# Kernel tuning notes

Hardware: AMD Instinct MI355X
Metric: run time of the kernel (lower is better)

The kernel has to match this reference:

```python
import jax, jax.numpy as jnp
import numpy as np

N, D = 100000, 256   # nodes, out_dim
E = N - 1            # chain dependency graph: gov[i]=i -> dep[i]=i+1
NEG = jnp.float32(-1e18)
LEAKY_SLOPE = 0.2    # __init__ alpha


def setup_inputs() -> dict:
    key = jax.random.key(0)
    k1, k2, k3 = jax.random.split(key, 3)
    x = jax.random.normal(k1, (N, D), dtype=jnp.float32)
    W = jax.random.normal(k2, (D, D), dtype=jnp.float32) / np.float32(np.sqrt(D))
    a = jax.random.normal(k3, (2 * D,), dtype=jnp.float32) / np.float32(np.sqrt(2 * D))
    gov = jnp.arange(E, dtype=jnp.int32)      # governors 0..N-2
    dep = jnp.arange(E, dtype=jnp.int32) + 1  # dependents 1..N-1 (each unique)
    return {"x": x, "W": W, "a": a, "gov": gov, "dep": dep}


def reference(x, W, a, gov, dep):
    n, d = x.shape
    h = x @ W.T                                   # [N, D]  W x_v for all nodes
    a_gov, a_dep = a[:d], a[d:]
    # per-edge score: attn_weight(cat(W x_gov, W x_dep))
    s = h[gov] @ a_gov + h[dep] @ a_dep           # [E]
    # original: masked_e = where(row > 0, row, -1e18); softmax over full row of N.
    # Non-edge entries are 0 -> masked to -1e18. In fp32 exp(-1e18 - rowmax)
    # underflows to 0 whenever rowmax > -1e18, so the dense softmax reduces to a
    # segment softmax over positive edge scores; if all row entries are masked,
    # softmax is uniform 1/N.
    sm = jnp.where(s > 0, s, NEG)
    rowmax = jax.ops.segment_max(sm, gov, num_segments=n)
    rowmax = jnp.maximum(rowmax, NEG)             # non-edge entries are -1e18
    ex = jnp.exp(sm - rowmax[gov])                # [E]
    deg = jax.ops.segment_sum(jnp.ones_like(s), gov, num_segments=n)
    denom = jax.ops.segment_sum(ex, gov, num_segments=n) \
          + (jnp.float32(n) - deg) * jnp.exp(NEG - rowmax)
    alpha = ex / denom[gov]                       # [E] attention coefficients
    # self_loop: h_dict[dep] = W x_gov (dep unique -> simple scatter-set); node 0 -> zeros
    base = jnp.zeros_like(h).at[dep].set(h[gov])
    # aggregation: h_dict[gov] += alpha * W x_dep
    out = base.at[gov].add(alpha[:, None] * h[dep])
    # is_dropout=False path: leakyrelu only (dropout is stochastic, eval mode)
    return jax.nn.leaky_relu(out, negative_slope=LEAKY_SLOPE)
```

## Files before the change

### kernel.cpp

```cpp
#include <hip/hip_runtime.h>

#define NR   100000
#define DD   256
#define BMO  62
#define HR   64
#define NCH  1613
#define GRID 256
#define LDA  72
#define LDH  264

typedef unsigned short u16;
typedef __bf16 bf16_t;
typedef bf16_t bf16x8 __attribute__((ext_vector_type(8)));
typedef float  f32x4  __attribute__((ext_vector_type(4)));
typedef u16    u16x8  __attribute__((ext_vector_type(8)));

__device__ __forceinline__ u16 f2bf(float f) {
    bf16_t b = (bf16_t)f;
    return __builtin_bit_cast(u16, b);
}
__device__ __forceinline__ float bf2f(u16 s) {
    unsigned u = ((unsigned)s) << 16;
    return __builtin_bit_cast(float, u);
}

__device__ __forceinline__ void block_sync() {
    asm volatile("s_waitcnt lgkmcnt(0)" ::: "memory");
    __builtin_amdgcn_s_barrier();
    asm volatile("" ::: "memory");
}

__global__ void uv_kernel(const float* __restrict__ W, const float* __restrict__ a,
                          float* __restrict__ uvp) {
    __shared__ double su[DD];
    __shared__ double sv[DD];
    const int k = blockIdx.x, j = threadIdx.x;
    double w = (double)W[j * DD + k];
    su[j] = w * (double)a[j];
    sv[j] = w * (double)a[DD + j];
    __syncthreads();
    for (int s = 128; s > 0; s >>= 1) {
        if (j < s) { su[j] += su[j + s]; sv[j] += sv[j + s]; }
        __syncthreads();
    }
    if (j == 0) { uvp[2 * k] = (float)su[0]; uvp[2 * k + 1] = (float)sv[0]; }
}

__device__ __forceinline__ f32x4 ldx4(const float* __restrict__ x, int grow, int col) {
    f32x4 r = (f32x4){0.f, 0.f, 0.f, 0.f};
    if ((unsigned)grow < (unsigned)NR)
        r = *(const f32x4*)(x + (size_t)(unsigned)grow * DD + col);
    return r;
}

__global__ __launch_bounds__(512, 1) void fused_kernel(
    const float* __restrict__ x, const float* __restrict__ W,
    const float* __restrict__ uvp, float* __restrict__ out) {

    __shared__ bf16_t lds_a[2][HR * LDA];
    __shared__ u16    h_lds[HR * LDH];
    __shared__ double g_lds[HR];
    __shared__ double d_lds[HR];
    __shared__ float  uv_lds[2 * DD];

    const int t    = threadIdx.x;
    const int lane = t & 63;
    const int wid  = t >> 6;
    const int frow = lane & 15;
    const int fk   = (lane >> 4) * 8;
    const int srow = t >> 3;
    const int scc  = (t & 7) * 8;

    uv_lds[t] = uvp[t];

    bf16x8 wfrag[16];
    #pragma unroll
    for (int kf = 0; kf < 8; ++kf) {
        #pragma unroll
        for (int nf = 0; nf < 2; ++nf) {
            const float* wp = W + (size_t)(wid * 32 + nf * 16 + frow) * DD + kf * 32 + fk;
            f32x4 w0 = *(const f32x4*)wp;
            f32x4 w1 = *(const f32x4*)(wp + 4);
            u16x8 b;
            #pragma unroll
            for (int e = 0; e < 4; ++e) {
                b[e]     = f2bf(w0[e]);
                b[e + 4] = f2bf(w1[e]);
            }
            wfrag[kf * 2 + nf] = __builtin_bit_cast(bf16x8, b);
        }
    }

    double gacc = 0.0, dacc = 0.0;
    f32x4 acc[4][2];
    f32x4 setA[4][2];

    auto issue2 = [&](f32x4* dst, int ch, int qi) {
        const int grow = ch * BMO - 1 + srow;
        const int col  = qi * 64 + scc;
        dst[0] = ldx4(x, grow, col);
        dst[1] = ldx4(x, grow, col + 4);
    };

    auto cw2 = [&](int buf, int qi, const f32x4* s) {
        const float* uvb = &uv_lds[(qi * 64 + scc) * 2];
        u16x8 b;
        double ag = 0.0, ad = 0.0;
        #pragma unroll
        for (int q = 0; q < 2; ++q)
            #pragma unroll
            for (int e = 0; e < 4; ++e) {
                const int idx = q * 4 + e;
                const float val = s[q][e];
                ag += (double)val * (double)uvb[2 * idx];
                ad += (double)val * (double)uvb[2 * idx + 1];
                b[idx] = f2bf(val);
            }
        *(u16x8*)(void*)&lds_a[buf][srow * LDA + scc] = b;
        gacc += ag; dacc += ad;
    };

    const int bid = blockIdx.x;
    const int c0 = (bid * NCH) / GRID;
    const int c1 = ((bid + 1) * NCH) / GRID;

    f32x4 T[2];
    issue2(T, c0, 0);
    issue2(setA[0], c0, 1);
    issue2(setA[1], c0, 2);
    issue2(setA[2], c0, 3);
    if (c0 + 1 < c1) issue2(setA[3], c0 + 1, 0);
    block_sync();
    cw2(0, 0, T);
    block_sync();

    for (int n = c0; n < c1; ++n) {
        #pragma unroll
        for (int m = 0; m < 4; ++m)
            #pragma unroll
            for (int nn = 0; nn < 2; ++nn)
                acc[m][nn] = (f32x4){0.f, 0.f, 0.f, 0.f};

        #pragma unroll
        for (int q = 0; q < 4; ++q) {
            const int qi   = (q + 1) & 3;
            const int cwCh = n + (q == 3);
            const int isCh = n + 1 + (q == 3);

            if (cwCh < c1) cw2((q + 1) & 1, qi, setA[q]);
            if (isCh < c1) issue2(setA[q], isCh, qi);

            {
                const bf16_t* ab = &lds_a[q & 1][0];
                #pragma unroll
                for (int kq = 0; kq < 2; ++kq) {
                    #pragma unroll
                    for (int nn = 0; nn < 2; ++nn) {
                        const bf16x8 bw = wfrag[(q * 2 + kq) * 2 + nn];
                        #pragma unroll
                        for (int m = 0; m < 4; ++m) {
                            bf16x8 am = *(const bf16x8*)(ab + (m * 16 + frow) * LDA + kq * 32 + fk);
                            acc[m][nn] = __builtin_amdgcn_mfma_f32_16x16x32_bf16(am, bw, acc[m][nn], 0, 0, 0);
                        }
                    }
                }
            }

            if (q == 2) {
                double ag = gacc, ad = dacc;
                ag += __shfl_down(ag, 4);  ad += __shfl_down(ad, 4);
                ag += __shfl_down(ag, 2);  ad += __shfl_down(ad, 2);
                ag += __shfl_down(ag, 1);  ad += __shfl_down(ad, 1);
                if ((t & 7) == 0) { g_lds[srow] = ag; d_lds[srow] = ad; }
                gacc = 0.0; dacc = 0.0;
            }
            block_sync();
        }

        #pragma unroll
        for (int m = 0; m < 4; ++m)
            #pragma unroll
            for (int nn = 0; nn < 2; ++nn)
                #pragma unroll
                for (int r = 0; r < 4; ++r)
                    h_lds[(m * 16 + (lane >> 4) * 4 + r) * LDH + wid * 32 + nn * 16 + frow] =
                        f2bf(acc[m][nn][r]);
        block_sync();

        const int m0 = n * BMO;
        const int rout = (NR - m0 < BMO) ? (NR - m0) : BMO;
        #pragma unroll
        for (int it = 0; it < 4; ++it) {
            const int item = t + it * 512;
            const int o = item >> 5;
            const int j = (item & 31) * 8;
            if (o < rout) {
                u16x8 hm = *(const u16x8*)(void*)&h_lds[o * LDH + j];
                u16x8 hp = *(const u16x8*)(void*)&h_lds[(o + 2) * LDH + j];
                const double s = g_lds[o + 1] + d_lds[o + 2];
                const float alpha = (s > 0.0) ? 1.0f : (1.0f / 100000.0f);
                f32x4 o0, o1;
                #pragma unroll
                for (int e = 0; e < 4; ++e) {
                    float p0 = bf2f(hm[e])     + alpha * bf2f(hp[e]);
                    float p1 = bf2f(hm[e + 4]) + alpha * bf2f(hp[e + 4]);
                    o0[e] = p0 > 0.f ? p0 : 0.2f * p0;
                    o1[e] = p1 > 0.f ? p1 : 0.2f * p1;
                }
                float* op = out + (size_t)(m0 + o) * DD + j;
                *(f32x4*)op       = o0;
                *(f32x4*)(op + 4) = o1;
            }
        }
        block_sync();
    }
}

extern "C" void kernel_launch(void* const* d_in, const int* in_sizes, int n_in,
                              void* d_out, int out_size, void* d_ws, size_t ws_size,
                              hipStream_t stream) {
    const float* x = (const float*)d_in[0];
    const float* W = (const float*)d_in[1];
    const float* a = (const float*)d_in[2];
    float* out = (float*)d_out;

    float* uvp = (float*)d_ws;

    uv_kernel<<<256, 256, 0, stream>>>(W, a, uvp);
    fused_kernel<<<GRID, 512, 0, stream>>>(x, W, uvp, out);
}
```

Measured before the change: 62.54 us.

## Compute epilogue from MFMA registers via shuffles, drop h LDS staging

The epilogue no longer stages the 64x256 h tile through LDS as bf16. It builds neighbor rows (row-1 and row+1) directly from the MFMA accumulators using cross-lane shuffles, with alpha precomputed into a small LDS array during the last k-quarter, and writes outputs with scalar nontemporal stores. This removes an LDS round trip and two barriers per chunk, keeps h in fp32, and frees LDS so GRID rises to 512 with launch_bounds no longer forcing one block per CU. The trade-off is scalar strided global stores (one float per lane per row) in place of 32-byte vector stores, which may hurt write coalescing.

```diff
diff --git a/kernel.cpp b/kernel.cpp
--- a/kernel.cpp
+++ b/kernel.cpp
@@ -5,9 +5,8 @@
 #define BMO  62
 #define HR   64
 #define NCH  1613
-#define GRID 256
+#define GRID 512
 #define LDA  72
-#define LDH  264
 
 typedef unsigned short u16;
 typedef __bf16 bf16_t;
@@ -18,10 +17,6 @@
 __device__ __forceinline__ u16 f2bf(float f) {
     bf16_t b = (bf16_t)f;
     return __builtin_bit_cast(u16, b);
-}
-__device__ __forceinline__ float bf2f(u16 s) {
-    unsigned u = ((unsigned)s) << 16;
-    return __builtin_bit_cast(float, u);
 }
 
 __device__ __forceinline__ void block_sync() {
@@ -53,21 +48,22 @@
     return r;
 }
 
-__global__ __launch_bounds__(512, 1) void fused_kernel(
+__global__ __launch_bounds__(512) void fused_kernel(
     const float* __restrict__ x, const float* __restrict__ W,
     const float* __restrict__ uvp, float* __restrict__ out) {
 
     __shared__ bf16_t lds_a[2][HR * LDA];
-    __shared__ u16    h_lds[HR * LDH];
     __shared__ double g_lds[HR];
     __shared__ double d_lds[HR];
+    __shared__ float  alpha_lds[HR];
     __shared__ float  uv_lds[2 * DD];
 
     const int t    = threadIdx.x;
     const int lane = t & 63;
+    const int hi   = lane >> 4;
     const int wid  = t >> 6;
     const int frow = lane & 15;
-    const int fk   = (lane >> 4) * 8;
+    const int fk   = hi * 8;
     const int srow = t >> 3;
     const int scc  = (t & 7) * 8;
 
@@ -174,45 +170,47 @@
                 if ((t & 7) == 0) { g_lds[srow] = ag; d_lds[srow] = ad; }
                 gacc = 0.0; dacc = 0.0;
             }
+            if (q == 3) {
+                if (t < HR) {
+                    float aval = 0.0f;
+                    if (t >= 1 && t <= 62)
+                        aval = (g_lds[t] + d_lds[t + 1] > 0.0) ? 1.0f : (1.0f / 100000.0f);
+                    alpha_lds[t] = aval;
+                }
+            }
             block_sync();
         }
 
-        #pragma unroll
-        for (int m = 0; m < 4; ++m)
-            #pragma unroll
-            for (int nn = 0; nn < 2; ++nn)
+        const int m0 = n * BMO;
+        #pragma unroll
+        for (int nn = 0; nn < 2; ++nn) {
+            const int col = wid * 32 + nn * 16 + frow;
+            float sh[4], sp[4];
+            #pragma unroll
+            for (int m = 0; m < 4; ++m) {
+                sh[m] = __shfl(acc[m][nn][3], (lane + 48) & 63, 64);
+                sp[m] = __shfl(acc[m][nn][0], (lane + 16) & 63, 64);
+            }
+            #pragma unroll
+            for (int m = 0; m < 4; ++m) {
+                const int wb = m * 16 + hi * 4;
+                const f32x4 av = *(const f32x4*)&alpha_lds[wb];
                 #pragma unroll
-                for (int r = 0; r < 4; ++r)
-                    h_lds[(m * 16 + (lane >> 4) * 4 + r) * LDH + wid * 32 + nn * 16 + frow] =
-                        f2bf(acc[m][nn][r]);
-        block_sync();
-
-        const int m0 = n * BMO;
-        const int rout = (NR - m0 < BMO) ? (NR - m0) : BMO;
-        #pragma unroll
-        for (int it = 0; it < 4; ++it) {
-            const int item = t + it * 512;
-            const int o = item >> 5;
-            const int j = (item & 31) * 8;
-            if (o < rout) {
-                u16x8 hm = *(const u16x8*)(void*)&h_lds[o * LDH + j];
-                u16x8 hp = *(const u16x8*)(void*)&h_lds[(o + 2) * LDH + j];
-                const double s = g_lds[o + 1] + d_lds[o + 2];
-                const float alpha = (s > 0.0) ? 1.0f : (1.0f / 100000.0f);
-                f32x4 o0, o1;
-                #pragma unroll
-                for (int e = 0; e < 4; ++e) {
-                    float p0 = bf2f(hm[e])     + alpha * bf2f(hp[e]);
-                    float p1 = bf2f(hm[e + 4]) + alpha * bf2f(hp[e + 4]);
-                    o0[e] = p0 > 0.f ? p0 : 0.2f * p0;
-                    o1[e] = p1 > 0.f ? p1 : 0.2f * p1;
+                for (int r = 0; r < 4; ++r) {
+                    float hmv, hpv;
+                    if (r > 0) hmv = acc[m][nn][r - 1];
+                    else       hmv = (hi > 0) ? sh[m] : (m > 0 ? sh[m - 1] : 0.0f);
+                    if (r < 3) hpv = acc[m][nn][r + 1];
+                    else       hpv = (hi < 3) ? sp[m] : (m < 3 ? sp[m + 1] : 0.0f);
+                    float res = hmv + av[r] * hpv;
+                    res = res > 0.0f ? res : 0.2f * res;
+                    const int w = wb + r;
+                    const int i = m0 + w - 1;
+                    if (w > 0 && w < 63 && i < NR)
+                        __builtin_nontemporal_store(res, out + (size_t)i * DD + col);
                 }
-                float* op = out + (size_t)(m0 + o) * DD + j;
-                *(f32x4*)op       = o0;
-                *(f32x4*)(op + 4) = o1;
             }
         }
-        block_sync();
     }
 }
 
```

Result: slower. 80.52 us (+28.7%).

## Stage full chunk per iteration with double-buffered LDS and fewer barriers

Applied to the files above, without the earlier changes.

Replaces the quarter-by-quarter interleaved pipeline (four barriers per chunk, LDA=72 half-tiles) with one full-width A tile per chunk. The next chunk's global loads are prefetched into registers while the current chunk is converted and multiplied. The h, g and d LDS buffers are double-buffered so the trailing barrier after the epilogue can be dropped, leaving two or three barriers per chunk. The cost is more LDS, more live registers (eight float4 prefetch registers plus the accumulators), and less fine-grained overlap between the loads and the MFMA work.

```diff
diff --git a/kernel.cpp b/kernel.cpp
--- a/kernel.cpp
+++ b/kernel.cpp
@@ -6,7 +6,7 @@
 #define HR   64
 #define NCH  1613
 #define GRID 256
-#define LDA  72
+#define LDA  264
 #define LDH  264
 
 typedef unsigned short u16;
@@ -58,9 +58,9 @@
     const float* __restrict__ uvp, float* __restrict__ out) {
 
     __shared__ bf16_t lds_a[2][HR * LDA];
-    __shared__ u16    h_lds[HR * LDH];
-    __shared__ double g_lds[HR];
-    __shared__ double d_lds[HR];
+    __shared__ u16    h_lds[2][HR * LDH];
+    __shared__ double g_lds[2][HR];
+    __shared__ double d_lds[2][HR];
     __shared__ float  uv_lds[2 * DD];
 
     const int t    = threadIdx.x;
@@ -91,50 +91,55 @@
         }
     }
 
-    double gacc = 0.0, dacc = 0.0;
     f32x4 acc[4][2];
-    f32x4 setA[4][2];
-
-    auto issue2 = [&](f32x4* dst, int ch, int qi) {
+    f32x4 set[8];
+
+    auto issue_all = [&](int ch) {
         const int grow = ch * BMO - 1 + srow;
-        const int col  = qi * 64 + scc;
-        dst[0] = ldx4(x, grow, col);
-        dst[1] = ldx4(x, grow, col + 4);
-    };
-
-    auto cw2 = [&](int buf, int qi, const f32x4* s) {
-        const float* uvb = &uv_lds[(qi * 64 + scc) * 2];
-        u16x8 b;
-        double ag = 0.0, ad = 0.0;
-        #pragma unroll
-        for (int q = 0; q < 2; ++q)
-            #pragma unroll
-            for (int e = 0; e < 4; ++e) {
-                const int idx = q * 4 + e;
-                const float val = s[q][e];
-                ag += (double)val * (double)uvb[2 * idx];
-                ad += (double)val * (double)uvb[2 * idx + 1];
-                b[idx] = f2bf(val);
-            }
-        *(u16x8*)(void*)&lds_a[buf][srow * LDA + scc] = b;
-        gacc += ag; dacc += ad;
+        #pragma unroll
+        for (int qi = 0; qi < 4; ++qi) {
+            set[qi * 2]     = ldx4(x, grow, qi * 64 + scc);
+            set[qi * 2 + 1] = ldx4(x, grow, qi * 64 + scc + 4);
+        }
     };
 
     const int bid = blockIdx.x;
     const int c0 = (bid * NCH) / GRID;
     const int c1 = ((bid + 1) * NCH) / GRID;
 
-    f32x4 T[2];
-    issue2(T, c0, 0);
-    issue2(setA[0], c0, 1);
-    issue2(setA[1], c0, 2);
-    issue2(setA[2], c0, 3);
-    if (c0 + 1 < c1) issue2(setA[3], c0 + 1, 0);
+    issue_all(c0);
     block_sync();
-    cw2(0, 0, T);
-    block_sync();
-
-    for (int n = c0; n < c1; ++n) {
+
+    int buf = 0;
+    for (int c = c0; c < c1; ++c) {
+        double gacc = 0.0, dacc = 0.0;
+        bf16_t* abuf = &lds_a[buf][0];
+        #pragma unroll
+        for (int qi = 0; qi < 4; ++qi) {
+            const float* uvb = &uv_lds[(qi * 64 + scc) * 2];
+            u16x8 b;
+            #pragma unroll
+            for (int q = 0; q < 2; ++q)
+                #pragma unroll
+                for (int e = 0; e < 4; ++e) {
+                    const int idx = q * 4 + e;
+                    const float val = set[qi * 2 + q][e];
+                    gacc += (double)val * (double)uvb[2 * idx];
+                    dacc += (double)val * (double)uvb[2 * idx + 1];
+                    b[idx] = f2bf(val);
+                }
+            *(u16x8*)(void*)&abuf[srow * LDA + qi * 64 + scc] = b;
+        }
+        {
+            double ag = gacc, ad = dacc;
+            ag += __shfl_down(ag, 4);  ad += __shfl_down(ad, 4);
+            ag += __shfl_down(ag, 2);  ad += __shfl_down(ad, 2);
+            ag += __shfl_down(ag, 1);  ad += __shfl_down(ad, 1);
+            if ((t & 7) == 0) { g_lds[buf][srow] = ag; d_lds[buf][srow] = ad; }
+        }
+        if (c + 1 < c1) issue_all(c + 1);
+        block_sync();
+
         #pragma unroll
         for (int m = 0; m < 4; ++m)
             #pragma unroll
@@ -142,39 +147,16 @@
                 acc[m][nn] = (f32x4){0.f, 0.f, 0.f, 0.f};
 
         #pragma unroll
-        for (int q = 0; q < 4; ++q) {
-            const int qi   = (q + 1) & 3;
-            const int cwCh = n + (q == 3);
-            const int isCh = n + 1 + (q == 3);
-
-            if (cwCh < c1) cw2((q + 1) & 1, qi, setA[q]);
-            if (isCh < c1) issue2(setA[q], isCh, qi);
-
-            {
-                const bf16_t* ab = &lds_a[q & 1][0];
-                #pragma unroll
-                for (int kq = 0; kq < 2; ++kq) {
-                    #pragma unroll
-                    for (int nn = 0; nn < 2; ++nn) {
-                        const bf16x8 bw = wfrag[(q * 2 + kq) * 2 + nn];
-                        #pragma unroll
-                        for (int m = 0; m < 4; ++m) {
-                            bf16x8 am = *(const bf16x8*)(ab + (m * 16 + frow) * LDA + kq * 32 + fk);
-                            acc[m][nn] = __builtin_amdgcn_mfma_f32_16x16x32_bf16(am, bw, acc[m][nn], 0, 0, 0);
-                        }
-                    }
+        for (int kq = 0; kq < 8; ++kq) {
+            #pragma unroll
+            for (int nn = 0; nn < 2; ++nn) {
+                const bf16x8 bw = wfrag[kq * 2 + nn];
+                #pragma unroll
+                for (int m = 0; m < 4; ++m) {
+                    bf16x8 am = *(const bf16x8*)(abuf + (m * 16 + frow) * LDA + kq * 32 + fk);
+                    acc[m][nn] = __builtin_amdgcn_mfma_f32_16x16x32_bf16(am, bw, acc[m][nn], 0, 0, 0);
                 }
             }
-
-            if (q == 2) {
-                double ag = gacc, ad = dacc;
-                ag += __shfl_down(ag, 4);  ad += __shfl_down(ad, 4);
-                ag += __shfl_down(ag, 2);  ad += __shfl_down(ad, 2);
-                ag += __shfl_down(ag, 1);  ad += __shfl_down(ad, 1);
-                if ((t & 7) == 0) { g_lds[srow] = ag; d_lds[srow] = ad; }
-                gacc = 0.0; dacc = 0.0;
-            }
-            block_sync();
         }
 
         #pragma unroll
@@ -183,11 +165,11 @@
             for (int nn = 0; nn < 2; ++nn)
                 #pragma unroll
                 for (int r = 0; r < 4; ++r)
-                    h_lds[(m * 16 + (lane >> 4) * 4 + r) * LDH + wid * 32 + nn * 16 + frow] =
+                    h_lds[buf][(m * 16 + (lane >> 4) * 4 + r) * LDH + wid * 32 + nn * 16 + frow] =
                         f2bf(acc[m][nn][r]);
         block_sync();
 
-        const int m0 = n * BMO;
+        const int m0 = c * BMO;
         const int rout = (NR - m0 < BMO) ? (NR - m0) : BMO;
         #pragma unroll
         for (int it = 0; it < 4; ++it) {
@@ -195,9 +177,9 @@
             const int o = item >> 5;
             const int j = (item & 31) * 8;
             if (o < rout) {
-                u16x8 hm = *(const u16x8*)(void*)&h_lds[o * LDH + j];
-                u16x8 hp = *(const u16x8*)(void*)&h_lds[(o + 2) * LDH + j];
-                const double s = g_lds[o + 1] + d_lds[o + 2];
+                u16x8 hm = *(const u16x8*)(void*)&h_lds[buf][o * LDH + j];
+                u16x8 hp = *(const u16x8*)(void*)&h_lds[buf][(o + 2) * LDH + j];
+                const double s = g_lds[buf][o + 1] + d_lds[buf][o + 2];
                 const float alpha = (s > 0.0) ? 1.0f : (1.0f / 100000.0f);
                 f32x4 o0, o1;
                 #pragma unroll
@@ -212,7 +194,7 @@
                 *(f32x4*)(op + 4) = o1;
             }
         }
-        block_sync();
+        buf ^= 1;
     }
 }
 
```

Result: faster. 55.19 us, median of 2 (-11.8%).
